# Optimization experiments

Hardware: AMD Instinct MI355X
Metric: run time of the kernel (lower is better)

## Reference

```python
import jax, jax.numpy as jnp
import numpy as np

BETA = 0.9
THRESHOLD = 1.0
SURROGATE_K = 25.0  # superspike slope

@jax.custom_vjp
def spike(u):
    # Heaviside forward, superspike surrogate gradient
    return (u > 0).astype(u.dtype)

def _spike_fwd(u):
    return spike(u), u

def _spike_bwd(u, g):
    return (g / jnp.square(1.0 + SURROGATE_K * jnp.abs(u)),)

spike.defvjp(_spike_fwd, _spike_bwd)

T, B = 512, 256
VIS_D, IMU_D, TRAJ_D = 256, 64, 64
HID, OUT = 256, 128
FUSE = VIS_D + IMU_D + TRAJ_D  # 384

def setup_inputs() -> dict:
    key = jax.random.key(0)
    ks = jax.random.split(key, 8)
    s_in = 1.0 / np.sqrt(FUSE)
    s_h = 1.0 / np.sqrt(HID)
    return {
        "vis_seq": jax.random.normal(ks[0], (T, B, VIS_D), jnp.float32),
        "imu_seq": jax.random.normal(ks[1], (T, B, IMU_D), jnp.float32),
        "traj_seq": jax.random.normal(ks[2], (T, B, TRAJ_D), jnp.float32),
        "W_in": jax.random.normal(ks[3], (FUSE, HID), jnp.float32) * s_in,
        "b_in": jnp.zeros((HID,), jnp.float32),
        "w_rec": jax.random.normal(ks[4], (HID,), jnp.float32) * 0.1,  # RLIF elementwise recurrent weight
        "W_head": jax.random.normal(ks[5], (HID, OUT), jnp.float32) * s_h,
        "b_head": jnp.zeros((OUT,), jnp.float32),
    }

def reference(vis_seq, imu_seq, traj_seq, W_in, b_in, w_rec, W_head, b_head):
    # fuse latents: [T, B, FUSE]
    fuse_seq = jnp.concatenate([vis_seq, imu_seq, traj_seq], axis=-1)
    # in_proj is time-invariant -> hoist the GEMM out of the scan (same math)
    x_proj = jnp.einsum("tbf,fh->tbh", fuse_seq, W_in) + b_in  # [T, B, HID]
    batch = imu_seq.shape[1]
    V0 = jnp.zeros((batch, HID), x_proj.dtype)
    S0 = jnp.zeros((batch, HID), x_proj.dtype)

    def step(carry, x_t):
        V, S = carry
        # recurrent LIF: leak + input + elementwise recurrent spike feedback
        V = BETA * V + x_t + w_rec * S
        S_new = spike(V - THRESHOLD)
        V = V - S_new * THRESHOLD  # soft reset
        return (V, S_new), S_new

    _, spikes_seq = jax.lax.scan(step, (V0, S0), x_proj)  # [T, B, HID]
    # head is also time-invariant -> single GEMM over the whole sequence
    logits_seq = jnp.einsum("tbh,ho->tbo", spikes_seq, W_head) + b_head  # [T, B, OUT]
    out = jnp.mean(logits_seq, axis=0)  # readout='mean' over time
    return out, logits_seq
```

## Files before the change

kernel.cpp:

```cpp
#include <hip/hip_runtime.h>
#include <hip/hip_bf16.h>
#include <cstdint>

#define T_LEN 512
#define B_SZ  256
#define HID   256
#define OUT   128
#define FUSE  384
#define MROWS (T_LEN * B_SZ)
#define FT    64

typedef _Float16 f16x8 __attribute__((ext_vector_type(8)));
typedef float f32x4 __attribute__((ext_vector_type(4)));

#define PRESC 4096.0f
#define S1    2048.0f
#define S1INV 4.8828125e-4f
#define C0    5.9604644775390625e-8f

#define EPSV  5e-5f

__device__ __forceinline__ void bar_plain() {
  asm volatile("s_barrier" ::: "memory");
}
__device__ __forceinline__ void bar_lds() {
  asm volatile("s_waitcnt lgkmcnt(0)\n\ts_barrier" ::: "memory");
}

__global__ __launch_bounds__(256) void prep_all(const float* __restrict__ Win,
                                                const float* __restrict__ Wh,
                                                _Float16* __restrict__ Bpack,
                                                _Float16* __restrict__ Wh3)
{
  int gid = blockIdx.x;
  if (gid < 96) {
    int id = gid * 256 + threadIdx.x;
    int img = id >> 10;
    int c = img >> 1, bc = img & 1;
    int slot = id & 1023;
    int s = slot >> 9, sub = (slot >> 6) & 7, pos = slot & 63;
    int fr = pos & 15, fq = pos >> 4;
    int n = bc * 128 + sub * 16 + fr;
    int k0 = c * 32 + fq * 8;
    f16x8 v;
#pragma unroll
    for (int j = 0; j < 8; ++j) {
      float w = Win[(size_t)(k0 + j) * HID + n] * PRESC;
      _Float16 h = (_Float16)w;
      v[j] = (s == 0) ? h : (_Float16)((w - (float)h) * S1);
    }
    *reinterpret_cast<f16x8*>(&Bpack[(size_t)img * 8192 + slot * 8]) = v;
  } else {
    int id = (gid - 96) * 256 + threadIdx.x;
    int n = id & 127, kk = (id >> 7) & 31, c = id >> 12;
    Wh3[((size_t)c * 128 + n) * 32 + kk] = (_Float16)Wh[(c * 32 + kk) * OUT + n];
  }
}

__global__ __launch_bounds__(512, 4) void k12_fused(
    const float* __restrict__ vis, const float* __restrict__ imu,
    const float* __restrict__ traj, const _Float16* __restrict__ Bpack,
    const float* __restrict__ bin, const float* __restrict__ wrec,
    uint32_t* __restrict__ sbits, float* __restrict__ scnt)
{
  __shared__ __align__(16) _Float16 Asl[4096];
  __shared__ float xt[FT][130];

  const int bid = blockIdx.x;
  const int b   = bid & 255;
  const int hh  = bid >> 8;
  const int tid = threadIdx.x;
  const int wid = tid >> 6, lane = tid & 63;
  const int wr = wid >> 2, wc = wid & 3;
  const int fr = lane & 15, fq = lane >> 4;

  const int arow = tid >> 2;
  const int ak   = (tid & 3) * 8;
  const int asub = arow >> 4;
  const int apos = (tid & 3) * 16 + (arow & 15);

  float V = 0.f, S = 0.f, cnt = 0.f, minm = 1e9f;
  const float wrv = (tid < 128) ? wrec[hh * 128 + tid] : 0.f;
  float bvv[2];
  bvv[0] = bin[hh * 128 + wc * 32 + fr];
  bvv[1] = bin[hh * 128 + wc * 32 + 16 + fr];

  float4 a0, a1;
  f16x8 pb0, pb1, pb2, pb3;

  auto loadA = [&](int tc, int c) {
    if (tid < 256) {
      size_t m = (size_t)(tc * FT + arow) * B_SZ + b;
      const float* src; size_t off;
      if (c < 8)       { src = vis;  off = m * 256 + c * 32 + ak; }
      else if (c < 10) { src = imu;  off = m * 64 + (c - 8) * 32 + ak; }
      else             { src = traj; off = m * 64 + (c - 10) * 32 + ak; }
      a0 = *reinterpret_cast<const float4*>(src + off);
      a1 = *reinterpret_cast<const float4*>(src + off + 4);
    }
  };
  auto loadB = [&](int c) {
    const _Float16* base = Bpack + (size_t)(c * 2 + hh) * 8192;
    pb0 = *reinterpret_cast<const f16x8*>(base + (wc * 2 + 0) * 512 + lane * 8);
    pb1 = *reinterpret_cast<const f16x8*>(base + (wc * 2 + 1) * 512 + lane * 8);
    pb2 = *reinterpret_cast<const f16x8*>(base + 4096 + (wc * 2 + 0) * 512 + lane * 8);
    pb3 = *reinterpret_cast<const f16x8*>(base + 4096 + (wc * 2 + 1) * 512 + lane * 8);
  };

  loadA(0, 0); loadB(0);

  for (int tc = 0; tc < 8; ++tc) {
    f32x4 acc0[2][2] = {};
    f32x4 acc1[2][2] = {};

#pragma unroll 1
    for (int c = 0; c < 12; ++c) {
      bar_plain();
      if (tid < 256) {
        float av[8] = {a0.x, a0.y, a0.z, a0.w, a1.x, a1.y, a1.z, a1.w};
        f16x8 vh, vl;
#pragma unroll
        for (int j = 0; j < 8; ++j) {
          float w = av[j] * PRESC;
          _Float16 h = (_Float16)w;
          vh[j] = h;
          vl[j] = (_Float16)((w - (float)h) * S1);
        }
        *reinterpret_cast<f16x8*>(&Asl[asub * 512 + apos * 8])        = vh;
        *reinterpret_cast<f16x8*>(&Asl[2048 + asub * 512 + apos * 8]) = vl;
      }
      bar_lds();
      f16x8 bh_0 = pb0, bh_1 = pb1, bl_0 = pb2, bl_1 = pb3;
      if (c + 1 < 12)      { loadA(tc, c + 1); loadB(c + 1); }
      else if (tc + 1 < 8) { loadA(tc + 1, 0); loadB(0); }

#pragma unroll
      for (int mf = 0; mf < 2; ++mf) {
        int sa = wr * 2 + mf;
        f16x8 ah = *reinterpret_cast<const f16x8*>(&Asl[sa * 512 + lane * 8]);
        f16x8 al = *reinterpret_cast<const f16x8*>(&Asl[2048 + sa * 512 + lane * 8]);
        acc0[mf][0] = __builtin_amdgcn_mfma_f32_16x16x32_f16(ah, bh_0, acc0[mf][0], 0, 0, 0);
        acc1[mf][0] = __builtin_amdgcn_mfma_f32_16x16x32_f16(ah, bl_0, acc1[mf][0], 0, 0, 0);
        acc1[mf][0] = __builtin_amdgcn_mfma_f32_16x16x32_f16(al, bh_0, acc1[mf][0], 0, 0, 0);
        acc0[mf][1] = __builtin_amdgcn_mfma_f32_16x16x32_f16(ah, bh_1, acc0[mf][1], 0, 0, 0);
        acc1[mf][1] = __builtin_amdgcn_mfma_f32_16x16x32_f16(ah, bl_1, acc1[mf][1], 0, 0, 0);
        acc1[mf][1] = __builtin_amdgcn_mfma_f32_16x16x32_f16(al, bh_1, acc1[mf][1], 0, 0, 0);
      }
    }

    __syncthreads();
#pragma unroll
    for (int mf = 0; mf < 2; ++mf)
#pragma unroll
      for (int nf = 0; nf < 2; ++nf) {
        int col = wc * 32 + nf * 16 + fr;
        int rbase = wr * 32 + mf * 16 + fq * 4;
#pragma unroll
        for (int r = 0; r < 4; ++r)
          xt[rbase + r][col] =
              (acc0[mf][nf][r] + acc1[mf][nf][r] * S1INV) * C0 + bvv[nf];
      }
    __syncthreads();

    if (tid < 128) {
#pragma unroll 1
      for (int u0 = 0; u0 < FT; u0 += 8) {
        float xv[8];
#pragma unroll
        for (int u = 0; u < 8; ++u) xv[u] = xt[u0 + u][tid];
#pragma unroll
        for (int u = 0; u < 8; ++u) {
          V = 0.9f * V + xv[u] + wrv * S;
          float d = V - 1.0f;
          float sn = (d > 0.0f) ? 1.0f : 0.0f;
          minm = fminf(minm, fabsf(d));
          V -= sn;
          cnt += sn;
          S = sn;
          unsigned long long mk = __ballot(sn > 0.5f);
          if (lane == 0) {
            int m = (tc * FT + u0 + u) * B_SZ + b;
            int wv = hh * 2 + wid;
            sbits[(size_t)m * 8 + wv * 2 + 0] = (uint32_t)(mk & 0xffffffffull);
            sbits[(size_t)m * 8 + wv * 2 + 1] = (uint32_t)(mk >> 32);
          }
        }
      }
    }
  }

  if (tid < 128)
    scnt[b * HID + hh * 128 + tid] = (minm < EPSV) ? (-cnt - 1.0f) : cnt;
}

#define FSL 12
__global__ __launch_bounds__(512) void k2_fix(
    const float* __restrict__ vis, const float* __restrict__ imu,
    const float* __restrict__ traj, const float* __restrict__ Win,
    const float* __restrict__ bin, const float* __restrict__ wrec,
    uint32_t* __restrict__ sbits, float* __restrict__ scnt)
{
  __shared__ __align__(16) float Wlds[FSL][392];
  __shared__ float xcol[FSL][521];
  __shared__ unsigned char spkb[FSL][516];
  __shared__ int dlist[256];
  __shared__ int nd;

  const int b = blockIdx.x;
  const int tid = threadIdx.x;
  if (tid == 0) nd = 0;
  __syncthreads();
  if (tid < 256) {
    if (scnt[b * HID + tid] < -0.5f) {
      int p = atomicAdd(&nd, 1);
      dlist[p] = tid;
    }
  }
  __syncthreads();
  const int nd0 = nd;
  if (nd0 == 0) return;

  const int t = tid;
  const size_t r = (size_t)t * B_SZ + b;

  for (int sb = 0; sb < nd0; sb += FSL) {
    const int nsb = min(FSL, nd0 - sb);

    for (int idx = tid; idx < FSL * 384; idx += 512) {
      int s = idx / 384, k = idx - s * 384;
      float w = 0.f;
      if (s < nsb) w = Win[(size_t)k * HID + dlist[sb + s]];
      Wlds[s][k] = w;
    }
    __syncthreads();

    float x[FSL];
#pragma unroll
    for (int s = 0; s < FSL; ++s) x[s] = 0.f;

#define SEG(SRC, LEN, DIM, WOFS)                                              \
    {                                                                         \
      const float* src = SRC + r * DIM;                                       \
      _Pragma("unroll 1")                                                     \
      for (int q = 0; q < LEN; q += 4) {                                      \
        float4 a0 = *reinterpret_cast<const float4*>(src + q * 4);            \
        float4 a1 = *reinterpret_cast<const float4*>(src + q * 4 + 4);        \
        float4 a2 = *reinterpret_cast<const float4*>(src + q * 4 + 8);        \
        float4 a3 = *reinterpret_cast<const float4*>(src + q * 4 + 12);       \
        _Pragma("unroll")                                                     \
        for (int s = 0; s < FSL; ++s) {                                       \
          float4 w = *reinterpret_cast<const float4*>(&Wlds[s][WOFS + q * 4]);\
          x[s] += a0.x * w.x; x[s] += a0.y * w.y;                             \
          x[s] += a0.z * w.z; x[s] += a0.w * w.w;                             \
        }                                                                     \
        _Pragma("unroll")                                                     \
        for (int s = 0; s < FSL; ++s) {                                       \
          float4 w = *reinterpret_cast<const float4*>(&Wlds[s][WOFS + q * 4 + 4]); \
          x[s] += a1.x * w.x; x[s] += a1.y * w.y;                             \
          x[s] += a1.z * w.z; x[s] += a1.w * w.w;                             \
        }                                                                     \
        _Pragma("unroll")                                                     \
        for (int s = 0; s < FSL; ++s) {                                       \
          float4 w = *reinterpret_cast<const float4*>(&Wlds[s][WOFS + q * 4 + 8]); \
          x[s] += a2.x * w.x; x[s] += a2.y * w.y;                             \
          x[s] += a2.z * w.z; x[s] += a2.w * w.w;                             \
        }                                                                     \
        _Pragma("unroll")                                                     \
        for (int s = 0; s < FSL; ++s) {                                       \
          float4 w = *reinterpret_cast<const float4*>(&Wlds[s][WOFS + q * 4 + 12]); \
          x[s] += a3.x * w.x; x[s] += a3.y * w.y;                             \
          x[s] += a3.z * w.z; x[s] += a3.w * w.w;                             \
        }                                                                     \
      }                                                                       \
    }

    SEG(vis,  64, 256, 0)
    SEG(imu,  16, 64,  256)
    SEG(traj, 16, 64,  320)
#undef SEG

#pragma unroll
    for (int s = 0; s < FSL; ++s) {
      if (s < nsb) xcol[s][t] = x[s] + bin[dlist[sb + s]];
    }
    __syncthreads();

    if (tid < nsb) {
      const int h = dlist[sb + tid];
      const float mywr = wrec[h];
      float V = 0.f, Sv = 0.f, cnt = 0.f;
#pragma unroll 1
      for (int tt = 0; tt < T_LEN; ++tt) {
        float xv = xcol[tid][tt];
        V = 0.9f * V + xv + mywr * Sv;
        float sn = (V - 1.0f > 0.0f) ? 1.0f : 0.0f;
        V -= sn;
        cnt += sn;
        Sv = sn;
        spkb[tid][tt] = (unsigned char)sn;
      }
      scnt[b * HID + h] = cnt;
    }
    __syncthreads();

    for (int p = tid; p < T_LEN * 8; p += 512) {
      int tt = p >> 3, wv = p & 7;
      uint32_t mc = 0, ms = 0;
      for (int j = 0; j < nsb; ++j) {
        int h = dlist[sb + j];
        if ((h >> 5) == wv) {
          uint32_t bit = 1u << (h & 31);
          mc |= bit;
          if (spkb[j][tt]) ms |= bit;
        }
      }
      if (mc) {
        size_t w = ((size_t)tt * B_SZ + b) * 8 + wv;
        sbits[w] = (sbits[w] & ~mc) | ms;
      }
    }
    __syncthreads();
  }
}

#define LDA 40
__global__ __launch_bounds__(256) void k3_logits(
    const uint32_t* __restrict__ sbits, const _Float16* __restrict__ Wh3,
    const float* __restrict__ bhead, float* __restrict__ logits)
{
  __shared__ __align__(16) _Float16 Sa[128][LDA];
  __shared__ __align__(16) _Float16 Wt[128][LDA];

  const int tid  = threadIdx.x;
  const int brow = blockIdx.x * 128;
  const int srow = tid >> 1, sks = (tid & 1) << 4;
  const int wid = tid >> 6, lane = tid & 63;
  const int wr = wid >> 1, wc = wid & 1;
  const int fr = lane & 15, fq = lane >> 4;

  f32x4 acc[4][4] = {};
  uint32_t wbits;
  uint4 wb0, wb1;

  auto loadS = [&](int c) { wbits = sbits[(size_t)(brow + srow) * 8 + c]; };
  auto loadW = [&](int c) {
    const _Float16* p = Wh3 + ((size_t)c * 128 + srow) * 32 + sks;
    wb0 = *reinterpret_cast<const uint4*>(p);
    wb1 = *reinterpret_cast<const uint4*>(p + 8);
  };

  loadS(0); loadW(0);

  for (int c = 0; c < 8; ++c) {
    __syncthreads();
    {
      f16x8 e0, e1;
#pragma unroll
      for (int j = 0; j < 8; ++j) {
        e0[j] = (_Float16)(float)((wbits >> (sks + j)) & 1u);
        e1[j] = (_Float16)(float)((wbits >> (sks + 8 + j)) & 1u);
      }
      *reinterpret_cast<f16x8*>(&Sa[srow][sks])     = e0;
      *reinterpret_cast<f16x8*>(&Sa[srow][sks + 8]) = e1;
    }
    *reinterpret_cast<uint4*>(&Wt[srow][sks])     = wb0;
    *reinterpret_cast<uint4*>(&Wt[srow][sks + 8]) = wb1;
    __syncthreads();
    if (c + 1 < 8) { loadS(c + 1); loadW(c + 1); }

    f16x8 wf[4];
#pragma unroll
    for (int nf = 0; nf < 4; ++nf)
      wf[nf] = *reinterpret_cast<const f16x8*>(&Wt[wc * 64 + nf * 16 + fr][fq * 8]);
#pragma unroll
    for (int mf = 0; mf < 4; ++mf) {
      f16x8 sf = *reinterpret_cast<const f16x8*>(&Sa[wr * 64 + mf * 16 + fr][fq * 8]);
#pragma unroll
      for (int nf = 0; nf < 4; ++nf)
        acc[mf][nf] = __builtin_amdgcn_mfma_f32_16x16x32_f16(sf, wf[nf], acc[mf][nf], 0, 0, 0);
    }
  }

#pragma unroll
  for (int mf = 0; mf < 4; ++mf)
#pragma unroll
    for (int nf = 0; nf < 4; ++nf) {
      int n = wc * 64 + nf * 16 + fr;
      float bv = bhead[n];
#pragma unroll
      for (int r = 0; r < 4; ++r) {
        int m = brow + wr * 64 + mf * 16 + fq * 4 + r;
        logits[(size_t)m * OUT + n] = acc[mf][nf][r] + bv;
      }
    }
}

__global__ __launch_bounds__(128) void k4_out(
    const float* __restrict__ scnt, const float* __restrict__ Whead,
    const float* __restrict__ bhead, float* __restrict__ outp)
{
  __shared__ float s[HID];
  const int b = blockIdx.x;
  const int o = threadIdx.x;
  s[o] = scnt[b * HID + o];
  s[o + 128] = scnt[b * HID + o + 128];
  __syncthreads();
  float acc = 0.f;
#pragma unroll 8
  for (int h = 0; h < HID; ++h) acc += s[h] * Whead[h * OUT + o];
  outp[b * OUT + o] = acc * (1.0f / (float)T_LEN) + bhead[o];
}

extern "C" void kernel_launch(void* const* d_in, const int* in_sizes, int n_in,
                              void* d_out, int out_size, void* d_ws, size_t ws_size,
                              hipStream_t stream)
{
  const float* vis   = (const float*)d_in[0];
  const float* imu   = (const float*)d_in[1];
  const float* traj  = (const float*)d_in[2];
  const float* Win   = (const float*)d_in[3];
  const float* bin   = (const float*)d_in[4];
  const float* wrec  = (const float*)d_in[5];
  const float* Whead = (const float*)d_in[6];
  const float* bhead = (const float*)d_in[7];

  float* outp   = (float*)d_out;
  float* logits = outp + B_SZ * OUT;

  char* ws = (char*)d_ws;
  const size_t SBITS_B = (size_t)MROWS * 8 * 4;
  const size_t SCNT_B  = (size_t)B_SZ * HID * 4;
  const size_t BPACK_B = (size_t)24 * 8192 * 2;
  uint32_t* sbits = (uint32_t*)ws;
  float*    scnt  = (float*)(ws + SBITS_B);
  _Float16* Bpack = (_Float16*)(ws + SBITS_B + SCNT_B);
  _Float16* Wh3   = (_Float16*)(ws + SBITS_B + SCNT_B + BPACK_B);

  prep_all  <<<dim3(224),         256, 0, stream>>>(Win, Whead, Bpack, Wh3);
  k12_fused <<<dim3(512),         512, 0, stream>>>(vis, imu, traj, Bpack, bin,
                                                    wrec, sbits, scnt);
  k2_fix    <<<dim3(B_SZ),        512, 0, stream>>>(vis, imu, traj, Win, bin,
                                                    wrec, sbits, scnt);
  k3_logits <<<dim3(MROWS / 128), 256, 0, stream>>>(sbits, Wh3, bhead, logits);
  k4_out    <<<dim3(B_SZ),        128, 0, stream>>>(scnt, Whead, bhead, outp);
}
```

Measured before the change: 272.6 us.

## Deepen global-load prefetch to four A chunks and two B chunks ahead

The fused in-projection GEMM loop now keeps four A-chunk register buffers and two B-fragment buffers in flight, using a flattened chunk index across time tiles, instead of prefetching only one chunk ahead. The aim is to hide global memory latency behind the MFMA work. The MFMA block is also wrapped in s_setprio to raise wave priority during matrix math. The extra register buffers raise VGPR pressure, which could reduce occupancy.

```diff
diff --git a/kernel.cpp b/kernel.cpp
--- a/kernel.cpp
+++ b/kernel.cpp
@@ -85,67 +85,103 @@
   bvv[0] = bin[hh * 128 + wc * 32 + fr];
   bvv[1] = bin[hh * 128 + wc * 32 + 16 + fr];
 
-  float4 a0, a1;
-  f16x8 pb0, pb1, pb2, pb3;
-
-  auto loadA = [&](int tc, int c) {
-    if (tid < 256) {
-      size_t m = (size_t)(tc * FT + arow) * B_SZ + b;
+  float4 aA0, aA1, aB0, aB1, aC0, aC1, aD0, aD1;
+  f16x8 pbE0, pbE1, pbE2, pbE3;
+  f16x8 pbO0, pbO1, pbO2, pbO3;
+
+  auto loadA = [&](int cc, float4& d0, float4& d1) {
+    if (tid < 256 && cc < 96) {
+      int tcc = cc / 12, c = cc - tcc * 12;
+      size_t m = (size_t)(tcc * FT + arow) * B_SZ + b;
       const float* src; size_t off;
       if (c < 8)       { src = vis;  off = m * 256 + c * 32 + ak; }
       else if (c < 10) { src = imu;  off = m * 64 + (c - 8) * 32 + ak; }
       else             { src = traj; off = m * 64 + (c - 10) * 32 + ak; }
-      a0 = *reinterpret_cast<const float4*>(src + off);
-      a1 = *reinterpret_cast<const float4*>(src + off + 4);
+      d0 = *reinterpret_cast<const float4*>(src + off);
+      d1 = *reinterpret_cast<const float4*>(src + off + 4);
     }
   };
-  auto loadB = [&](int c) {
-    const _Float16* base = Bpack + (size_t)(c * 2 + hh) * 8192;
-    pb0 = *reinterpret_cast<const f16x8*>(base + (wc * 2 + 0) * 512 + lane * 8);
-    pb1 = *reinterpret_cast<const f16x8*>(base + (wc * 2 + 1) * 512 + lane * 8);
-    pb2 = *reinterpret_cast<const f16x8*>(base + 4096 + (wc * 2 + 0) * 512 + lane * 8);
-    pb3 = *reinterpret_cast<const f16x8*>(base + 4096 + (wc * 2 + 1) * 512 + lane * 8);
+  auto loadB = [&](int cc, f16x8& d0, f16x8& d1, f16x8& d2, f16x8& d3) {
+    if (cc < 96) {
+      int c = cc - (cc / 12) * 12;
+      const _Float16* base = Bpack + (size_t)(c * 2 + hh) * 8192;
+      d0 = *reinterpret_cast<const f16x8*>(base + (wc * 2 + 0) * 512 + lane * 8);
+      d1 = *reinterpret_cast<const f16x8*>(base + (wc * 2 + 1) * 512 + lane * 8);
+      d2 = *reinterpret_cast<const f16x8*>(base + 4096 + (wc * 2 + 0) * 512 + lane * 8);
+      d3 = *reinterpret_cast<const f16x8*>(base + 4096 + (wc * 2 + 1) * 512 + lane * 8);
+    }
   };
 
-  loadA(0, 0); loadB(0);
+  auto stage = [&](const float4& s0, const float4& s1) {
+    if (tid < 256) {
+      float av[8] = {s0.x, s0.y, s0.z, s0.w, s1.x, s1.y, s1.z, s1.w};
+      f16x8 vh, vl;
+#pragma unroll
+      for (int j = 0; j < 8; ++j) {
+        float w = av[j] * PRESC;
+        _Float16 h = (_Float16)w;
+        vh[j] = h;
+        vl[j] = (_Float16)((w - (float)h) * S1);
+      }
+      *reinterpret_cast<f16x8*>(&Asl[asub * 512 + apos * 8])        = vh;
+      *reinterpret_cast<f16x8*>(&Asl[2048 + asub * 512 + apos * 8]) = vl;
+    }
+  };
+
+  f32x4 acc0[2][2];
+  f32x4 acc1[2][2];
+
+  auto mma = [&](f16x8 bh_0, f16x8 bh_1, f16x8 bl_0, f16x8 bl_1) {
+    __builtin_amdgcn_s_setprio(1);
+#pragma unroll
+    for (int mf = 0; mf < 2; ++mf) {
+      int sa = wr * 2 + mf;
+      f16x8 ah = *reinterpret_cast<const f16x8*>(&Asl[sa * 512 + lane * 8]);
+      f16x8 al = *reinterpret_cast<const f16x8*>(&Asl[2048 + sa * 512 + lane * 8]);
+      acc0[mf][0] = __builtin_amdgcn_mfma_f32_16x16x32_f16(ah, bh_0, acc0[mf][0], 0, 0, 0);
+      acc1[mf][0] = __builtin_amdgcn_mfma_f32_16x16x32_f16(ah, bl_0, acc1[mf][0], 0, 0, 0);
+      acc1[mf][0] = __builtin_amdgcn_mfma_f32_16x16x32_f16(al, bh_0, acc1[mf][0], 0, 0, 0);
+      acc0[mf][1] = __builtin_amdgcn_mfma_f32_16x16x32_f16(ah, bh_1, acc0[mf][1], 0, 0, 0);
+      acc1[mf][1] = __builtin_amdgcn_mfma_f32_16x16x32_f16(ah, bl_1, acc1[mf][1], 0, 0, 0);
+      acc1[mf][1] = __builtin_amdgcn_mfma_f32_16x16x32_f16(al, bh_1, acc1[mf][1], 0, 0, 0);
+    }
+    __builtin_amdgcn_s_setprio(0);
+  };
+
+  loadA(0, aA0, aA1);
+  loadA(1, aB0, aB1);
+  loadA(2, aC0, aC1);
+  loadA(3, aD0, aD1);
+  loadB(0, pbE0, pbE1, pbE2, pbE3);
+  loadB(1, pbO0, pbO1, pbO2, pbO3);
+
+#define CHUNK(S0, S1, P0, P1, P2, P3, CC)                                     \
+  {                                                                           \
+    bar_plain();                         \
+    stage(S0, S1);                                                            \
+    loadA((CC) + 4, S0, S1);                              \
+    bar_lds();                                         \
+    f16x8 t0 = P0, t1 = P1, t2 = P2, t3 = P3;                                 \
+    loadB((CC) + 2, P0, P1, P2, P3);                      \
+    mma(t0, t1, t2, t3);                                                      \
+  }
 
   for (int tc = 0; tc < 8; ++tc) {
-    f32x4 acc0[2][2] = {};
-    f32x4 acc1[2][2] = {};
+#pragma unroll
+    for (int mf = 0; mf < 2; ++mf)
+#pragma unroll
+      for (int nf = 0; nf < 2; ++nf) {
+        acc0[mf][nf] = (f32x4){0.f, 0.f, 0.f, 0.f};
+        acc1[mf][nf] = (f32x4){0.f, 0.f, 0.f, 0.f};
+      }
 
 #pragma unroll 1
-    for (int c = 0; c < 12; ++c) {
-      bar_plain();
-      if (tid < 256) {
-        float av[8] = {a0.x, a0.y, a0.z, a0.w, a1.x, a1.y, a1.z, a1.w};
-        f16x8 vh, vl;
-#pragma unroll
-        for (int j = 0; j < 8; ++j) {
-          float w = av[j] * PRESC;
-          _Float16 h = (_Float16)w;
-          vh[j] = h;
-          vl[j] = (_Float16)((w - (float)h) * S1);
-        }
-        *reinterpret_cast<f16x8*>(&Asl[asub * 512 + apos * 8])        = vh;
-        *reinterpret_cast<f16x8*>(&Asl[2048 + asub * 512 + apos * 8]) = vl;
-      }
-      bar_lds();
-      f16x8 bh_0 = pb0, bh_1 = pb1, bl_0 = pb2, bl_1 = pb3;
-      if (c + 1 < 12)      { loadA(tc, c + 1); loadB(c + 1); }
-      else if (tc + 1 < 8) { loadA(tc + 1, 0); loadB(0); }
-
-#pragma unroll
-      for (int mf = 0; mf < 2; ++mf) {
-        int sa = wr * 2 + mf;
-        f16x8 ah = *reinterpret_cast<const f16x8*>(&Asl[sa * 512 + lane * 8]);
-        f16x8 al = *reinterpret_cast<const f16x8*>(&Asl[2048 + sa * 512 + lane * 8]);
-        acc0[mf][0] = __builtin_amdgcn_mfma_f32_16x16x32_f16(ah, bh_0, acc0[mf][0], 0, 0, 0);
-        acc1[mf][0] = __builtin_amdgcn_mfma_f32_16x16x32_f16(ah, bl_0, acc1[mf][0], 0, 0, 0);
-        acc1[mf][0] = __builtin_amdgcn_mfma_f32_16x16x32_f16(al, bh_0, acc1[mf][0], 0, 0, 0);
-        acc0[mf][1] = __builtin_amdgcn_mfma_f32_16x16x32_f16(ah, bh_1, acc0[mf][1], 0, 0, 0);
-        acc1[mf][1] = __builtin_amdgcn_mfma_f32_16x16x32_f16(ah, bl_1, acc1[mf][1], 0, 0, 0);
-        acc1[mf][1] = __builtin_amdgcn_mfma_f32_16x16x32_f16(al, bh_1, acc1[mf][1], 0, 0, 0);
-      }
+    for (int i = 0; i < 3; ++i) {
+      const int cc0 = tc * 12 + 4 * i;
+      CHUNK(aA0, aA1, pbE0, pbE1, pbE2, pbE3, cc0 + 0)
+      CHUNK(aB0, aB1, pbO0, pbO1, pbO2, pbO3, cc0 + 1)
+      CHUNK(aC0, aC1, pbE0, pbE1, pbE2, pbE3, cc0 + 2)
+      CHUNK(aD0, aD1, pbO0, pbO1, pbO2, pbO3, cc0 + 3)
     }
 
     __syncthreads();
@@ -192,6 +228,7 @@
   if (tid < 128)
     scnt[b * HID + hh * 128 + tid] = (minm < EPSV) ? (-cnt - 1.0f) : cnt;
 }
+#undef CHUNK
 
 #define FSL 12
 __global__ __launch_bounds__(512) void k2_fix(
```

Measured after the change: 376.4 us. +38.0%, slower.
